# Performance work log

Hardware: AMD Instinct MI355X
Metric: run time of the kernel (lower is better)

The kernel has to match this reference:

```python
import jax, jax.numpy as jnp
import numpy as np
import math

L, H, HD, D = 3, 8, 32, 256
TN, TE = 4, 3


def _layer_norm(x, g, b, eps=1e-5):
    m = jnp.mean(x, axis=-1, keepdims=True)
    v = jnp.var(x, axis=-1, keepdims=True)
    return (x - m) / jnp.sqrt(v + eps) * g + b


def _typed_transform(xh, W, types):
    # xh: [M, H, d], W: [T, H, d, d], types: [M] int -> per-row type-specific matmul
    out = jnp.zeros_like(xh)
    for t in range(W.shape[0]):
        y = jnp.einsum('mhd,hde->mhe', xh, W[t])
        out = jnp.where((types == t)[:, None, None], y, out)
    return out


def setup_inputs() -> dict:
    N, E = 20000, 320000
    key = jax.random.key(0)
    ks = jax.random.split(key, 16)
    inp = {}
    inp['x'] = jax.random.normal(ks[0], (N, D), dtype=jnp.float32)
    inp['edge_index'] = jax.random.randint(ks[1], (2, E), 0, N)
    inp['edge_type'] = jax.random.randint(ks[2], (E,), 0, TE)
    inp['node_type'] = jax.random.randint(ks[3], (N,), 0, TN)
    inp['W_Q'] = jax.random.normal(ks[4], (L, TN, H, HD, HD), dtype=jnp.float32) * 0.02
    inp['W_K'] = jax.random.normal(ks[5], (L, TN, H, HD, HD), dtype=jnp.float32) * 0.02
    inp['W_V'] = jax.random.normal(ks[6], (L, TN, H, HD, HD), dtype=jnp.float32) * 0.02
    inp['W_E'] = jax.random.normal(ks[7], (L, TE, H, HD, HD), dtype=jnp.float32) * 0.02
    inp['mu'] = jnp.ones((L, H, TE), dtype=jnp.float32)
    inp['Wo'] = jax.random.normal(ks[8], (L, D, D), dtype=jnp.float32) * 0.02
    inp['bo'] = jnp.zeros((L, D), dtype=jnp.float32)
    inp['ln1_g'] = jnp.ones((L, D), dtype=jnp.float32)
    inp['ln1_b'] = jnp.zeros((L, D), dtype=jnp.float32)
    inp['ln2_g'] = jnp.ones((L, D), dtype=jnp.float32)
    inp['ln2_b'] = jnp.zeros((L, D), dtype=jnp.float32)
    inp['w1'] = jax.random.normal(ks[9], (L, D, 4 * D), dtype=jnp.float32) * 0.02
    inp['b1'] = jnp.zeros((L, 4 * D), dtype=jnp.float32)
    inp['w2'] = jax.random.normal(ks[10], (L, 4 * D, D), dtype=jnp.float32) * 0.02
    inp['b2'] = jnp.zeros((L, D), dtype=jnp.float32)
    inp['out_g'] = jnp.ones((D,), dtype=jnp.float32)
    inp['out_b'] = jnp.zeros((D,), dtype=jnp.float32)
    return inp


def reference(x, edge_index, edge_type, node_type, W_Q, W_K, W_V, W_E, mu,
              Wo, bo, ln1_g, ln1_b, ln2_g, ln2_b, w1, b1, w2, b2, out_g, out_b):
    N = x.shape[0]
    src, dst = edge_index[0], edge_index[1]
    scale = math.sqrt(HD)
    for l in range(L):
        xh = x.reshape(N, H, HD)
        Q = _typed_transform(xh, W_Q[l], node_type)
        K = _typed_transform(xh, W_K[l], node_type)
        V = _typed_transform(xh, W_V[l], node_type)
        q_dst = Q[dst]                                  # [E,H,hd]
        kt = _typed_transform(K[src], W_E[l], edge_type)  # per-edge-type transform
        scores = jnp.sum(q_dst * kt, axis=-1) / scale   # [E,H]
        scores = scores * mu[l].T[edge_type]            # mu[l]: [H,TE] -> [E,H]
        m = jax.ops.segment_max(scores, dst, num_segments=N)
        m = jnp.maximum(m, -1e9)                        # match torch -1e9 init
        e = jnp.exp(scores - m[dst])
        s = jax.ops.segment_sum(e, dst, num_segments=N)
        w = e / (s[dst] + 1e-10)
        agg = jax.ops.segment_sum(V[src] * w[..., None], dst, num_segments=N)
        attn = agg.reshape(N, D) @ Wo[l] + bo[l]
        x = _layer_norm(x + attn, ln1_g[l], ln1_b[l])
        h = jax.nn.gelu(x @ w1[l] + b1[l], approximate=False) @ w2[l] + b2[l]
        x = _layer_norm(x + h, ln2_g[l], ln2_b[l])
    return _layer_norm(x, out_g, out_b)
```

## Files before the change

### kernel.cpp

```cpp
#include <hip/hip_runtime.h>
#include <hip/hip_fp8.h>
#include <math.h>

#define HDIM 32
#define NHEAD 8
#define DMODEL 256
#define NTYPE 4
#define ETYPE 3
#define NLAYER 3

typedef unsigned short u16;
typedef unsigned char u8;
typedef __bf16 bf16x8 __attribute__((ext_vector_type(8)));
typedef float f32x4 __attribute__((ext_vector_type(4)));

__device__ __forceinline__ u16 f2bf(float f) {
  union { float f; unsigned u; } v; v.f = f;
  unsigned r = v.u + 0x7FFF + ((v.u >> 16) & 1);
  return (u16)(r >> 16);
}
__device__ __forceinline__ float bf2f(u16 b) {
  union { unsigned u; float f; } v; v.u = (unsigned)b << 16; return v.f;
}
__device__ __forceinline__ u8 f2fp8(float v) {
  __hip_fp8_e4m3 t(v); return (u8)t.__x;
}
__device__ __forceinline__ float fp82f(unsigned b) {
  __hip_fp8_e4m3 t; t.__x = (__hip_fp8_storage_t)b; return (float)t;
}

__device__ __forceinline__ float gelu_f(float v) {
  float u = 0.7978845608028654f * v * (1.f + 0.044715f * v * v);
  float e = __expf(-2.f * fabsf(u));
  float th = (1.f - e) / (1.f + e);
  th = copysignf(th, u);
  return 0.5f * v * (1.f + th);
}

#define GLDS16(g, l)                                              \
  __builtin_amdgcn_global_load_lds(                               \
      (const __attribute__((address_space(1))) void*)(g),         \
      (__attribute__((address_space(3))) void*)(l), 16, 0, 0)

__global__ void count_deg_kernel(const int* __restrict__ dst, int* __restrict__ deg, int E) {
  int tid = blockIdx.x * 256 + threadIdx.x;
  if (tid < E) atomicAdd(&deg[dst[tid]], 1);
}

__global__ __launch_bounds__(1024) void scan_kernel(const int* __restrict__ deg,
                                                    int* __restrict__ off, int n) {
  __shared__ int part[1024];
  int t = threadIdx.x;
  int chunk = (n + 1023) >> 10;
  int base = t * chunk;
  int s = 0;
  for (int i = 0; i < chunk; ++i) {
    int idx = base + i;
    if (idx < n) s += deg[idx];
  }
  part[t] = s;
  __syncthreads();
  for (int o = 1; o < 1024; o <<= 1) {
    int v = (t >= o) ? part[t - o] : 0;
    __syncthreads();
    part[t] += v;
    __syncthreads();
  }
  int run = part[t] - s;
  for (int i = 0; i < chunk; ++i) {
    int idx = base + i;
    if (idx < n) { off[idx] = run; run += deg[idx]; }
  }
  if (t == 1023) off[n] = part[1023];
}

__global__ void scatter_kernel(const int* __restrict__ src, const int* __restrict__ dst,
                               const int* __restrict__ etype,
                               const int* __restrict__ off, int* __restrict__ cursor,
                               int* __restrict__ csr_src,
                               int* __restrict__ csr_et, int E) {
  int tid = blockIdx.x * 256 + threadIdx.x;
  if (tid < E) {
    int d = dst[tid];
    int p = atomicAdd(&cursor[d], 1);
    int pos = off[d] + p;
    csr_src[pos] = src[tid];
    csr_et[pos] = etype[tid];
  }
}

__global__ void tcount_kernel(const int* __restrict__ nt, int* __restrict__ tcnt, int N) {
  __shared__ int h[NTYPE];
  int t = threadIdx.x;
  if (t < NTYPE) h[t] = 0;
  __syncthreads();
  int tid = blockIdx.x * 256 + t;
  if (tid < N) atomicAdd(&h[nt[tid]], 1);
  __syncthreads();
  if (t < NTYPE && h[t] > 0) atomicAdd(&tcnt[t], h[t]);
}

__global__ void tscan_kernel(const int* __restrict__ tcnt, int* __restrict__ toff,
                             int* __restrict__ tile_off) {
  if (threadIdx.x == 0 && blockIdx.x == 0) {
    int o = 0, to = 0;
    for (int t = 0; t < NTYPE; ++t) {
      toff[t] = o; tile_off[t] = to;
      o += tcnt[t]; to += (tcnt[t] + 63) >> 6;
    }
    toff[NTYPE] = o; tile_off[NTYPE] = to;
  }
}

__global__ void tscatter_kernel(const int* __restrict__ nt, const int* __restrict__ toff,
                                int* __restrict__ tcur, int* __restrict__ tidx, int N) {
  int tid = blockIdx.x * 256 + threadIdx.x;
  int lane = threadIdx.x & 63;
  int ty = (tid < N) ? nt[tid] : -1;
  unsigned long long lt_mask = (lane == 63) ? 0x7FFFFFFFFFFFFFFFull
                                            : ((1ull << lane) - 1);
#pragma unroll
  for (int t4 = 0; t4 < NTYPE; ++t4) {
    unsigned long long mask = __ballot(ty == t4);
    if (mask == 0) continue;
    int first = __builtin_ctzll(mask);
    int cnt = __popcll(mask);
    int base = 0;
    if (lane == first) base = atomicAdd(&tcur[t4], cnt);
    base = __shfl(base, first, 64);
    if (ty == t4) {
      int rank = __popcll(mask & lt_mask);
      tidx[toff[t4] + base + rank] = tid;
    }
  }
}

__global__ void xconv_kernel(const float* __restrict__ x, float* __restrict__ xbuf,
                             u16* __restrict__ xb, int n4) {
  int i = blockIdx.x * 256 + threadIdx.x;
  if (i < n4) {
    float4 v = ((const float4*)x)[i];
    ((float4*)xbuf)[i] = v;
    ushort4 o = { f2bf(v.x), f2bf(v.y), f2bf(v.z), f2bf(v.w) };
    ((ushort4*)xb)[i] = o;
  }
}

__global__ __launch_bounds__(256) void wprep_kernel(
    const float* __restrict__ W_Q, const float* __restrict__ W_K,
    const float* __restrict__ W_V, const float* __restrict__ W_E,
    u16* __restrict__ wqkvb) {
  int b = blockIdx.x;
  int h = b & 7, tt = (b >> 3) & 3, l = b >> 5;
  __shared__ float wq[1056];
  __shared__ float we[3][1024];
  int t = threadIdx.x;
  const float* WQp = W_Q + (((size_t)l * NTYPE + tt) * NHEAD + h) * 1024;
  for (int i = t; i < 1024; i += 256) wq[(i >> 5) * 33 + (i & 31)] = WQp[i];
  for (int et = 0; et < ETYPE; ++et) {
    const float* WEp = W_E + (((size_t)l * ETYPE + et) * NHEAD + h) * 1024;
    for (int i = t; i < 1024; i += 256) we[et][i] = WEp[i];
  }
  __syncthreads();
  const float* WKp = W_K + (((size_t)l * NTYPE + tt) * NHEAD + h) * 1024;
  const float* WVp = W_V + (((size_t)l * NTYPE + tt) * NHEAD + h) * 1024;
  u16* out = wqkvb + (size_t)b * 5120;
  for (int i = t; i < 1024; i += 256) {
    int col = i >> 5, k = i & 31;
    out[i] = f2bf(WKp[k * 32 + col]);
    out[1024 + i] = f2bf(WVp[k * 32 + col]);
#pragma unroll
    for (int et = 0; et < ETYPE; ++et) {
      float a = 0.f;
#pragma unroll
      for (int j = 0; j < 32; ++j) a += wq[k * 33 + j] * we[et][col * 32 + j];
      out[(2 + et) * 1024 + i] = f2bf(a);
    }
  }
}

__global__ __launch_bounds__(256) void qkv_mfma(
    const u16* __restrict__ xb, const int* __restrict__ tidx,
    const int* __restrict__ toff, const int* __restrict__ tile_off,
    const u16* __restrict__ wqkvb_l,
    u8* __restrict__ Kb8, u8* __restrict__ Vb8, u16* __restrict__ Qeb) {
  __shared__ u16 smem[10240];
  int bx = blockIdx.x, h = blockIdx.y;
  if (bx >= tile_off[NTYPE]) return;
  int ty = 0;
  while (bx >= tile_off[ty + 1]) ++ty;
  int lt = bx - tile_off[ty];
  int base = toff[ty] + lt * 64;
  int cnt = min(64, toff[ty + 1] - toff[ty] - lt * 64);
  int t = threadIdx.x;
  {
    int row = ((t >> 6) << 4) | (t & 15);
    int q = (t >> 4) & 3;
    int node = tidx[base + min(row, cnt - 1)];
    *(uint4*)&smem[t * 8] =
        *(const uint4*)&xb[(size_t)node * 256 + h * 32 + q * 8];
  }
  const u16* wsrc = wqkvb_l + ((size_t)ty * NHEAD + h) * 5120;
  for (int dc = t; dc < 640; dc += 256) {
    int mt = dc >> 7, wi = dc & 127, slot = wi >> 5, colx = wi & 31;
    *(uint4*)&smem[2048 + dc * 8] = *(const uint4*)&wsrc[(mt * 128 + colx * 4 + slot) * 8];
  }
  __syncthreads();

  int lane = t & 63, w = t >> 6;
  int m = lane & 15, q = lane >> 4;
  bf16x8 af = *(const bf16x8*)&smem[w * 512 + q * 128 + m * 8];
  f32x4 acc[5][2];
#pragma unroll
  for (int mt = 0; mt < 5; ++mt)
#pragma unroll
    for (int c = 0; c < 2; ++c) {
      bf16x8 bf = *(const bf16x8*)&smem[2048 + mt * 1024 + q * 256 + (c * 16 + m) * 8];
      acc[mt][c] = __builtin_amdgcn_mfma_f32_16x16x32_bf16(af, bf, (f32x4){0.f, 0.f, 0.f, 0.f}, 0, 0, 0);
    }
  __syncthreads();
#pragma unroll
  for (int mt = 0; mt < 5; ++mt)
#pragma unroll
    for (int c = 0; c < 2; ++c)
#pragma unroll
      for (int r = 0; r < 4; ++r)
        smem[mt * 2048 + (w * 16 + q * 4 + r) * 32 + c * 16 + m] = f2bf(acc[mt][c][r]);
  __syncthreads();
  {
    int row = t >> 2, q4 = t & 3;
    if (row < cnt) {
      int node = tidx[base + row];
      {
        const u16* sp = &smem[row * 32 + q4 * 8];
        unsigned long long pk = 0;
#pragma unroll
        for (int j = 0; j < 8; ++j)
          pk |= (unsigned long long)f2fp8(bf2f(sp[j])) << (8 * j);
        *(unsigned long long*)&Kb8[(size_t)node * 256 + h * 32 + q4 * 8] = pk;
      }
      {
        const u16* sp = &smem[2048 + row * 32 + q4 * 8];
        unsigned long long pk = 0;
#pragma unroll
        for (int j = 0; j < 8; ++j)
          pk |= (unsigned long long)f2fp8(bf2f(sp[j])) << (8 * j);
        *(unsigned long long*)&Vb8[(size_t)node * 256 + h * 32 + q4 * 8] = pk;
      }
#pragma unroll
      for (int et = 0; et < ETYPE; ++et)
        *(uint4*)&Qeb[((size_t)node * ETYPE + et) * 256 + h * 32 + q4 * 8] =
            *(const uint4*)&smem[(2 + et) * 2048 + row * 32 + q4 * 8];
    }
  }
}

__global__ __launch_bounds__(256) void agg_kernel(
    const int* __restrict__ off, const int* __restrict__ csr_src,
    const int* __restrict__ csr_et, const u16* __restrict__ Qeb,
    const u8* __restrict__ Kb8, const float* __restrict__ mu,
    const u8* __restrict__ Vb8, u16* __restrict__ aggb) {
  __shared__ float sacc[4][256];
  __shared__ float sssum[4][8];
  int n = blockIdx.x;
  int t = threadIdx.x;
  int g = t >> 6;
  int l = t & 63;
  int d0 = l * 4;
  int h = l >> 3;

  float4 q0, q1, q2;
  {
    const u16* qp = Qeb + (size_t)n * ETYPE * 256 + d0;
    ushort4 a = *(const ushort4*)(qp);
    ushort4 b = *(const ushort4*)(qp + 256);
    ushort4 c = *(const ushort4*)(qp + 512);
    q0 = make_float4(bf2f(a.x), bf2f(a.y), bf2f(a.z), bf2f(a.w));
    q1 = make_float4(bf2f(b.x), bf2f(b.y), bf2f(b.z), bf2f(b.w));
    q2 = make_float4(bf2f(c.x), bf2f(c.y), bf2f(c.z), bf2f(c.w));
  }
  const float sc = 0.17677669529663687f;
  float mu0 = sc * mu[h * ETYPE + 0];
  float mu1 = sc * mu[h * ETYPE + 1];
  float mu2 = sc * mu[h * ETYPE + 2];

  int s0 = off[n], s1 = off[n + 1];
  float a0 = 0.f, a1 = 0.f, a2 = 0.f, a3 = 0.f, ssum = 0.f;
  for (int k = s0 + g; k < s1; k += 4) {
    int sn = csr_src[k];
    int et = csr_et[k];
    unsigned k4 = *(const unsigned*)(Kb8 + (size_t)sn * 256 + d0);
    float4 qe = (et == 0) ? q0 : (et == 1) ? q1 : q2;
    float mue = (et == 0) ? mu0 : (et == 1) ? mu1 : mu2;
    float p = fp82f(k4 & 0xffu) * qe.x + fp82f((k4 >> 8) & 0xffu) * qe.y
            + fp82f((k4 >> 16) & 0xffu) * qe.z + fp82f((k4 >> 24) & 0xffu) * qe.w;
    p += __shfl_xor(p, 1, 64);
    p += __shfl_xor(p, 2, 64);
    p += __shfl_xor(p, 4, 64);
    float e = __expf(p * mue);
    unsigned v4 = *(const unsigned*)(Vb8 + (size_t)sn * 256 + d0);
    a0 += e * fp82f(v4 & 0xffu);
    a1 += e * fp82f((v4 >> 8) & 0xffu);
    a2 += e * fp82f((v4 >> 16) & 0xffu);
    a3 += e * fp82f((v4 >> 24) & 0xffu);
    ssum += e;
  }
  *(float4*)&sacc[g][d0] = make_float4(a0, a1, a2, a3);
  if ((l & 7) == 0) sssum[g][h] = ssum;
  __syncthreads();
  int hh = t >> 5;
  float tot = sacc[0][t] + sacc[1][t] + sacc[2][t] + sacc[3][t];
  float st = sssum[0][hh] + sssum[1][hh] + sssum[2][hh] + sssum[3][hh];
  aggb[(size_t)n * 256 + t] = f2bf(tot / (st + 1e-10f));
}

__global__ __launch_bounds__(256) void convT_kernel(const float* __restrict__ W,
                                                    u16* __restrict__ Wt, int K, int Nc) {
  __shared__ float tile[32][33];
  int bk = blockIdx.y * 32, bn = blockIdx.x * 32;
  const float* Wz = W + (size_t)blockIdx.z * K * Nc;
  u16* Wtz = Wt + (size_t)blockIdx.z * K * Nc;
  int tx = threadIdx.x & 31, ty = threadIdx.x >> 5;
  for (int r = ty; r < 32; r += 8)
    tile[r][tx] = Wz[(size_t)(bk + r) * Nc + bn + tx];
  __syncthreads();
  for (int r = ty; r < 32; r += 8)
    Wtz[(size_t)(bn + r) * K + bk + tx] = f2bf(tile[tx][r]);
}

template <int GELU, int BN>
__global__ __launch_bounds__(256) void gemm_mfma(
    const u16* __restrict__ A, const u16* __restrict__ Bt,
    const float* __restrict__ bias, u16* __restrict__ Cb,
    int M, int K, int Nc) {
  constexpr int MJ = BN / 32;
  __shared__ u16 As[128 * 64];
  __shared__ u16 Bs[BN * 64];
  const int t = threadIdx.x;
  const int lane = t & 63;
  const int w = t >> 6;

  const int nwg = gridDim.x * gridDim.y;
  const int lin = blockIdx.y * gridDim.x + blockIdx.x;
  const int qq = nwg >> 3, rr = nwg & 7;
  const int xcd = lin & 7, pos = lin >> 3;
  const int nl = (xcd < rr ? xcd * (qq + 1) : rr * (qq + 1) + (xcd - rr) * qq) + pos;
  const int row0 = (nl / gridDim.x) * 128;
  const int col0 = (nl % gridDim.x) * BN;

  const int wm = (w >> 1) * 64, wn = (w & 1) * (BN / 2);

  f32x4 acc[4][MJ] = {};
  const int sr = lane >> 2;
  const int sk = (lane & 3) * 8;

  for (int k0 = 0; k0 < K; k0 += 64) {
#pragma unroll
    for (int half = 0; half < 2; ++half) {
#pragma unroll
      for (int c = 0; c < 2; ++c) {
        const int chunk = w * 2 + c;
        const int r = chunk * 16 + sr;
        int ra = row0 + r; if (ra >= M) ra = M - 1;
        GLDS16(A + (size_t)ra * K + k0 + half * 32 + sk,
               &As[((half * 8 + chunk) * 64 + lane) * 8]);
        if (BN == 128) {
          GLDS16(Bt + (size_t)(col0 + r) * K + k0 + half * 32 + sk,
                 &Bs[((half * 8 + chunk) * 64 + lane) * 8]);
        }
      }
      if (BN == 64) {
        const int r = w * 16 + sr;
        GLDS16(Bt + (size_t)(col0 + r) * K + k0 + half * 32 + sk,
               &Bs[((half * 4 + w) * 64 + lane) * 8]);
      }
    }
    __syncthreads();
    const int ko = (lane >> 4) * 8;
    const int lr = lane & 15;
#pragma unroll
    for (int half = 0; half < 2; ++half) {
      bf16x8 af[4], bfr[MJ];
      const int ab = half * 8 * 512;
      const int bb = half * (BN == 128 ? 8 : 4) * 512;
#pragma unroll
      for (int i = 0; i < 4; ++i)
        af[i] = *(const bf16x8*)&As[ab + ((wm >> 4) + i) * 512 + lr * 32 + ko];
#pragma unroll
      for (int j = 0; j < MJ; ++j)
        bfr[j] = *(const bf16x8*)&Bs[bb + ((wn >> 4) + j) * 512 + lr * 32 + ko];
#pragma unroll
      for (int i = 0; i < 4; ++i)
#pragma unroll
        for (int j = 0; j < MJ; ++j)
          acc[i][j] = __builtin_amdgcn_mfma_f32_16x16x32_bf16(af[i], bfr[j], acc[i][j], 0, 0, 0);
    }
    __syncthreads();
  }

  const int lc = lane & 15;
  const int lrow = (lane >> 4) * 4;
  float bv[MJ];
#pragma unroll
  for (int j = 0; j < MJ; ++j) bv[j] = bias[col0 + wn + j * 16 + lc];
#pragma unroll
  for (int i = 0; i < 4; ++i) {
#pragma unroll
    for (int r = 0; r < 4; ++r) {
      int gr = row0 + wm + i * 16 + lrow + r;
      if (gr >= M) continue;
#pragma unroll
      for (int j = 0; j < MJ; ++j) {
        int gc = col0 + wn + j * 16 + lc;
        float v = acc[i][j][r] + bv[j];
        if (GELU) v = gelu_f(v);
        Cb[(size_t)gr * Nc + gc] = f2bf(v);
      }
    }
  }
}

__global__ __launch_bounds__(256) void ln_kernel(
    const float* __restrict__ xin, const u16* __restrict__ res,
    const float* __restrict__ g, const float* __restrict__ b,
    float* __restrict__ out, u16* __restrict__ outb, int N) {
  int row = blockIdx.x * 4 + (threadIdx.x >> 6);
  if (row >= N) return;
  int l = threadIdx.x & 63;
  size_t base = (size_t)row * 256 + l * 4;
  float4 r4 = *(const float4*)&xin[base];
  if (res) {
    ushort4 rb = *(const ushort4*)&res[base];
    r4.x += bf2f(rb.x); r4.y += bf2f(rb.y);
    r4.z += bf2f(rb.z); r4.w += bf2f(rb.w);
  }
  float s = r4.x + r4.y + r4.z + r4.w;
  for (int o = 32; o > 0; o >>= 1) s += __shfl_xor(s, o, 64);
  float m = s * (1.f / 256.f);
  float dx = r4.x - m, dy = r4.y - m, dz = r4.z - m, dw = r4.w - m;
  float s2 = dx * dx + dy * dy + dz * dz + dw * dw;
  for (int o = 32; o > 0; o >>= 1) s2 += __shfl_xor(s2, o, 64);
  float inv = rsqrtf(s2 * (1.f / 256.f) + 1e-5f);
  float4 g4 = *(const float4*)&g[l * 4];
  float4 b4 = *(const float4*)&b[l * 4];
  float4 o4 = { dx * inv * g4.x + b4.x, dy * inv * g4.y + b4.y,
                dz * inv * g4.z + b4.z, dw * inv * g4.w + b4.w };
  *(float4*)&out[base] = o4;
  if (outb) {
    ushort4 ob = { f2bf(o4.x), f2bf(o4.y), f2bf(o4.z), f2bf(o4.w) };
    *(ushort4*)&outb[base] = ob;
  }
}

extern "C" void kernel_launch(void* const* d_in, const int* in_sizes, int n_in,
                              void* d_out, int out_size, void* d_ws, size_t ws_size,
                              hipStream_t stream) {
  const float* x_in   = (const float*)d_in[0];
  const int*   ei     = (const int*)d_in[1];
  const int*   etype  = (const int*)d_in[2];
  const int*   ntype  = (const int*)d_in[3];
  const float* W_Q    = (const float*)d_in[4];
  const float* W_K    = (const float*)d_in[5];
  const float* W_V    = (const float*)d_in[6];
  const float* W_E    = (const float*)d_in[7];
  const float* mu     = (const float*)d_in[8];
  const float* Wo     = (const float*)d_in[9];
  const float* bo     = (const float*)d_in[10];
  const float* ln1g   = (const float*)d_in[11];
  const float* ln1b   = (const float*)d_in[12];
  const float* ln2g   = (const float*)d_in[13];
  const float* ln2b   = (const float*)d_in[14];
  const float* w1     = (const float*)d_in[15];
  const float* b1     = (const float*)d_in[16];
  const float* w2     = (const float*)d_in[17];
  const float* b2     = (const float*)d_in[18];
  const float* outg   = (const float*)d_in[19];
  const float* outb   = (const float*)d_in[20];

  const int N = in_sizes[0] / DMODEL;
  const int E = in_sizes[1] / 2;
  const int* src = ei;
  const int* dst = ei + E;

  const size_t NF = (size_t)N * DMODEL;
  const size_t EH = (size_t)E * NHEAD;

  float* f      = (float*)d_ws;
  float* xbuf   = f;
  float* scores = f + NF;
  u16*   fout   = (u16*)(f + NF + EH);
  u16*   xb     = fout + NF;
  u16*   Qeb    = xb + NF;
  u16*   h1b    = Qeb;
  u16*   aggb   = Qeb + 3 * NF;
  u8*    Kb8    = (u8*)(aggb + NF);
  u8*    Vb8    = Kb8 + NF;
  u16*   wqkvb  = (u16*)(Vb8 + NF);
  u16*   Wot    = wqkvb + (size_t)NLAYER * NTYPE * NHEAD * 5120;
  u16*   w1t    = Wot + 3 * 65536;
  u16*   w2t    = w1t + 3 * 262144;
  int*   ip     = (int*)(w2t + 3 * 262144);
  int*   off    = ip;
  int*   csr_src= off + (N + 1);
  int*   csr_dst= csr_src + E;
  int*   csr_et = csr_dst + E;
  int*   cursor = csr_et + E;
  int*   tidx   = cursor + N;
  int*   toff   = tidx + N;
  int*   tile_off = toff + (NTYPE + 1);
  int*   tcnt   = tile_off + (NTYPE + 1);
  int*   tcur   = tcnt + NTYPE;
  (void)scores; (void)csr_dst;

  hipMemsetAsync(cursor, 0, (size_t)N * sizeof(int), stream);
  hipMemsetAsync(tcnt, 0, 2 * NTYPE * sizeof(int), stream);
  count_deg_kernel<<<(E + 255) / 256, 256, 0, stream>>>(dst, cursor, E);
  scan_kernel<<<1, 1024, 0, stream>>>(cursor, off, N);
  hipMemsetAsync(cursor, 0, (size_t)N * sizeof(int), stream);
  scatter_kernel<<<(E + 255) / 256, 256, 0, stream>>>(
      src, dst, etype, off, cursor, csr_src, csr_et, E);
  tcount_kernel<<<(N + 255) / 256, 256, 0, stream>>>(ntype, tcnt, N);
  tscan_kernel<<<1, 64, 0, stream>>>(tcnt, toff, tile_off);
  tscatter_kernel<<<(N + 255) / 256, 256, 0, stream>>>(ntype, toff, tcur, tidx, N);

  wprep_kernel<<<NLAYER * NTYPE * NHEAD, 256, 0, stream>>>(W_Q, W_K, W_V, W_E, wqkvb);
  convT_kernel<<<dim3(DMODEL / 32, DMODEL / 32, NLAYER), 256, 0, stream>>>(
      Wo, Wot, DMODEL, DMODEL);
  convT_kernel<<<dim3(4 * DMODEL / 32, DMODEL / 32, NLAYER), 256, 0, stream>>>(
      w1, w1t, DMODEL, 4 * DMODEL);
  convT_kernel<<<dim3(DMODEL / 32, 4 * DMODEL / 32, NLAYER), 256, 0, stream>>>(
      w2, w2t, 4 * DMODEL, DMODEL);

  xconv_kernel<<<(int)((NF / 4 + 255) / 256), 256, 0, stream>>>(
      x_in, xbuf, xb, (int)(NF / 4));

  const int gm = (N + 127) / 128;
  const int lng = (N + 3) / 4;
  const int qtiles = (N + 63) / 64 + NTYPE;
  for (int l = 0; l < NLAYER; ++l) {
    qkv_mfma<<<dim3(qtiles, NHEAD), 256, 0, stream>>>(
        xb, tidx, toff, tile_off,
        wqkvb + (size_t)l * NTYPE * NHEAD * 5120, Kb8, Vb8, Qeb);
    agg_kernel<<<N, 256, 0, stream>>>(off, csr_src, csr_et, Qeb, Kb8,
        mu + (size_t)l * NHEAD * ETYPE, Vb8, aggb);

    gemm_mfma<0, 128><<<dim3(DMODEL / 128, gm), 256, 0, stream>>>(
        aggb, Wot + (size_t)l * 65536, bo + (size_t)l * DMODEL,
        fout, N, DMODEL, DMODEL);
    ln_kernel<<<lng, 256, 0, stream>>>(xbuf, fout,
        ln1g + (size_t)l * DMODEL, ln1b + (size_t)l * DMODEL, xbuf, xb, N);
    gemm_mfma<1, 128><<<dim3(4 * DMODEL / 128, gm), 256, 0, stream>>>(
        xb, w1t + (size_t)l * 262144, b1 + (size_t)l * 4 * DMODEL,
        h1b, N, DMODEL, 4 * DMODEL);
    gemm_mfma<0, 128><<<dim3(DMODEL / 128, gm), 256, 0, stream>>>(
        h1b, w2t + (size_t)l * 262144, b2 + (size_t)l * DMODEL,
        fout, N, 4 * DMODEL, DMODEL);
    ln_kernel<<<lng, 256, 0, stream>>>(xbuf, fout,
        ln2g + (size_t)l * DMODEL, ln2b + (size_t)l * DMODEL, xbuf, xb, N);
  }

  ln_kernel<<<lng, 256, 0, stream>>>(xbuf, nullptr, outg, outb, (float*)d_out, nullptr, N);
}
```

Before: 706.4 us.

## Assign one wavefront per node in aggregation and use packed FP8 conversion

The aggregation kernel now gives each 64-lane wavefront its own destination node, four nodes per block, in place of one node per block split four ways over edges. This drops the shared-memory reduction and the block barrier. Each wave accumulates its node's edges serially and writes normalized bf16 output directly. Per-byte FP8 decodes are replaced with the packed cvt_pk_f32_fp8 builtin, at the cost of less memory-level parallelism per node on high-degree nodes.

```diff
diff --git a/kernel.cpp b/kernel.cpp
--- a/kernel.cpp
+++ b/kernel.cpp
@@ -13,6 +13,7 @@
 typedef unsigned char u8;
 typedef __bf16 bf16x8 __attribute__((ext_vector_type(8)));
 typedef float f32x4 __attribute__((ext_vector_type(4)));
+typedef float f32x2 __attribute__((ext_vector_type(2)));
 
 __device__ __forceinline__ u16 f2bf(float f) {
   union { float f; unsigned u; } v; v.f = f;
@@ -27,6 +28,11 @@
 }
 __device__ __forceinline__ float fp82f(unsigned b) {
   __hip_fp8_e4m3 t; t.__x = (__hip_fp8_storage_t)b; return (float)t;
+}
+__device__ __forceinline__ float4 fp8x4_f32(unsigned v) {
+  f32x2 lo = __builtin_amdgcn_cvt_pk_f32_fp8((int)v, false);
+  f32x2 hi = __builtin_amdgcn_cvt_pk_f32_fp8((int)v, true);
+  return make_float4(lo[0], lo[1], hi[0], hi[1]);
 }
 
 __device__ __forceinline__ float gelu_f(float v) {
@@ -259,13 +265,10 @@
     const int* __restrict__ off, const int* __restrict__ csr_src,
     const int* __restrict__ csr_et, const u16* __restrict__ Qeb,
     const u8* __restrict__ Kb8, const float* __restrict__ mu,
-    const u8* __restrict__ Vb8, u16* __restrict__ aggb) {
-  __shared__ float sacc[4][256];
-  __shared__ float sssum[4][8];
-  int n = blockIdx.x;
-  int t = threadIdx.x;
-  int g = t >> 6;
-  int l = t & 63;
+    const u8* __restrict__ Vb8, u16* __restrict__ aggb, int N) {
+  int n = blockIdx.x * 4 + (threadIdx.x >> 6);
+  if (n >= N) return;
+  int l = threadIdx.x & 63;
   int d0 = l * 4;
   int h = l >> 3;
 
@@ -286,32 +289,29 @@
 
   int s0 = off[n], s1 = off[n + 1];
   float a0 = 0.f, a1 = 0.f, a2 = 0.f, a3 = 0.f, ssum = 0.f;
-  for (int k = s0 + g; k < s1; k += 4) {
+  for (int k = s0; k < s1; ++k) {
     int sn = csr_src[k];
     int et = csr_et[k];
     unsigned k4 = *(const unsigned*)(Kb8 + (size_t)sn * 256 + d0);
+    float4 kf = fp8x4_f32(k4);
     float4 qe = (et == 0) ? q0 : (et == 1) ? q1 : q2;
     float mue = (et == 0) ? mu0 : (et == 1) ? mu1 : mu2;
-    float p = fp82f(k4 & 0xffu) * qe.x + fp82f((k4 >> 8) & 0xffu) * qe.y
-            + fp82f((k4 >> 16) & 0xffu) * qe.z + fp82f((k4 >> 24) & 0xffu) * qe.w;
+    float p = kf.x * qe.x + kf.y * qe.y + kf.z * qe.z + kf.w * qe.w;
     p += __shfl_xor(p, 1, 64);
     p += __shfl_xor(p, 2, 64);
     p += __shfl_xor(p, 4, 64);
     float e = __expf(p * mue);
     unsigned v4 = *(const unsigned*)(Vb8 + (size_t)sn * 256 + d0);
-    a0 += e * fp82f(v4 & 0xffu);
-    a1 += e * fp82f((v4 >> 8) & 0xffu);
-    a2 += e * fp82f((v4 >> 16) & 0xffu);
-    a3 += e * fp82f((v4 >> 24) & 0xffu);
+    float4 vf = fp8x4_f32(v4);
+    a0 += e * vf.x;
+    a1 += e * vf.y;
+    a2 += e * vf.z;
+    a3 += e * vf.w;
     ssum += e;
   }
-  *(float4*)&sacc[g][d0] = make_float4(a0, a1, a2, a3);
-  if ((l & 7) == 0) sssum[g][h] = ssum;
-  __syncthreads();
-  int hh = t >> 5;
-  float tot = sacc[0][t] + sacc[1][t] + sacc[2][t] + sacc[3][t];
-  float st = sssum[0][hh] + sssum[1][hh] + sssum[2][hh] + sssum[3][hh];
-  aggb[(size_t)n * 256 + t] = f2bf(tot / (st + 1e-10f));
+  float inv = 1.f / (ssum + 1e-10f);
+  ushort4 o = { f2bf(a0 * inv), f2bf(a1 * inv), f2bf(a2 * inv), f2bf(a3 * inv) };
+  *(ushort4*)&aggb[(size_t)n * 256 + d0] = o;
 }
 
 __global__ __launch_bounds__(256) void convT_kernel(const float* __restrict__ W,
@@ -541,8 +541,8 @@
     qkv_mfma<<<dim3(qtiles, NHEAD), 256, 0, stream>>>(
         xb, tidx, toff, tile_off,
         wqkvb + (size_t)l * NTYPE * NHEAD * 5120, Kb8, Vb8, Qeb);
-    agg_kernel<<<N, 256, 0, stream>>>(off, csr_src, csr_et, Qeb, Kb8,
-        mu + (size_t)l * NHEAD * ETYPE, Vb8, aggb);
+    agg_kernel<<<lng, 256, 0, stream>>>(off, csr_src, csr_et, Qeb, Kb8,
+        mu + (size_t)l * NHEAD * ETYPE, Vb8, aggb, N);
 
     gemm_mfma<0, 128><<<dim3(DMODEL / 128, gm), 256, 0, stream>>>(
         aggb, Wot + (size_t)l * 65536, bo + (size_t)l * DMODEL,
```

After: 700.4 us. About the same (-0.9%).
